# Kernel optimization log

Measured on AMD Instinct MI355X. Metric: run time of the kernel, lower is better.

The kernel has to match this reference:

```python
import jax, jax.numpy as jnp
import numpy as np

THRESHOLD_IOU = 0.8  # forward default in the original module


def setup_inputs() -> dict:
    key = jax.random.key(0)
    k1, k2, k3, k4 = jax.random.split(key, 4)
    N = M = 16
    H = W = 768
    # Binary masks (the original zeroes pixels to 0.0 and tests >0 via torch.where)
    masks_a = (jax.random.uniform(k1, (N, H, W)) > 0.6).astype(jnp.float32)
    masks_b = (jax.random.uniform(k2, (M, H, W)) > 0.6).astype(jnp.float32)
    # Make a few masks identical across labels so the IoU>threshold (suppression)
    # branch is exercised, not just the partial-overlap zeroing branch.
    masks_b = masks_b.at[:4].set(masks_a[:4])
    scores_a = jax.random.uniform(k3, (N,))
    scores_b = jax.random.uniform(k4, (M,))
    return {"masks_a": masks_a, "masks_b": masks_b,
            "scores_a": scores_a, "scores_b": scores_b}


def _overlap_filter(masks_a, masks_b, scores_a, scores_b, thr):
    # Sequential pairwise IoU + overlap zeroing, faithful to the original
    # nested product(enumerate(masks), enumerate(other_masks)) loop order
    # (i outer, j inner), where each pair sees masks already modified by
    # earlier pairs. Pruning ("keep") is applied after the loop; here it is
    # represented with static shapes as keep flags + zeroed-out rows.
    N, H, W = masks_a.shape
    M = masks_b.shape[0]
    P = H * W
    A0 = masks_a.reshape(N, P)
    B0 = masks_b.reshape(M, P)

    def body(carry, k):
        A, B, fi, fj = carry
        i = k // M
        j = k % M
        a = A[i]  # [P]
        b = B[j]  # [P]
        abin = a > 0
        bbin = b > 0
        inter = abin & bbin
        inter_sum = jnp.sum(inter.astype(jnp.float32))
        union_sum = jnp.sum((abin | bbin).astype(jnp.float32))
        iou = inter_sum / jnp.maximum(union_sum, 1.0)
        a_wins = scores_a[i] > scores_b[j]
        suppress = iou > thr                 # mark whole loser mask for removal
        zero_case = (iou > 0) & ~suppress    # zero overlapped pixels of loser
        b_new = jnp.where(zero_case & a_wins & inter, 0.0, b)
        a_new = jnp.where(zero_case & (~a_wins) & inter, 0.0, a)
        A = A.at[i].set(a_new)
        B = B.at[j].set(b_new)
        fj = fj.at[j].set(fj[j] | (suppress & a_wins))
        fi = fi.at[i].set(fi[i] | (suppress & ~a_wins))
        return (A, B, fi, fj), None

    fi0 = jnp.zeros(N, dtype=bool)
    fj0 = jnp.zeros(M, dtype=bool)
    (A, B, fi, fj), _ = jax.lax.scan(body, (A0, B0, fi0, fj0), jnp.arange(N * M))
    keep_a = ~fi
    keep_b = ~fj
    A = jnp.where(keep_a[:, None], A, 0.0)
    B = jnp.where(keep_b[:, None], B, 0.0)
    return A.reshape(N, H, W), B.reshape(M, H, W), keep_a, keep_b


def reference(masks_a, masks_b, scores_a, scores_b):
    return _overlap_filter(masks_a, masks_b, scores_a, scores_b, THRESHOLD_IOU)
```

## Files before the change

kernel.cpp:

```cpp
#include <hip/hip_runtime.h>
#include <stdint.h>

#define NM 16
#define HW_P 589824
#define U8PM 9216
#define C4PM 4608
#define F4PM 147456
#define F4PT 2359296
#define PT 512
#define NG 8
#define EWG 64

typedef unsigned long long u64;
typedef float vf4 __attribute__((ext_vector_type(4)));


__device__ __forceinline__ unsigned aload(const unsigned* p) {
    return __hip_atomic_load(p, __ATOMIC_RELAXED, __HIP_MEMORY_SCOPE_AGENT);
}
__device__ __forceinline__ void astore(unsigned* p, unsigned v) {
    __hip_atomic_store(p, v, __ATOMIC_RELAXED, __HIP_MEMORY_SCOPE_AGENT);
}
__device__ __forceinline__ unsigned afadd(unsigned* p, unsigned v) {
    return __hip_atomic_fetch_add(p, v, __ATOMIC_RELAXED, __HIP_MEMORY_SCOPE_AGENT);
}

#define LOAD16_SC0(dst, addr) \
    asm volatile("global_load_dwordx4 %0, %1, off sc0" : "=v"(dst) : "v"(addr))

__device__ __forceinline__ uint32_t spread4(uint32_t x) {
    uint32_t t = (x | (x << 12)) & 0x000F000Fu;
    t = (t | (t << 6)) & 0x03030303u;
    t = (t | (t << 3)) & 0x11111111u;
    return t;
}

__global__ __launch_bounds__(256) void binarize_kernel(
    const float* __restrict__ ma, const float* __restrict__ mb,
    uint32_t* __restrict__ bitsA, uint32_t* __restrict__ bitsB,
    uint4* __restrict__ meta4)
{
    if (blockIdx.x == 0) {
        uint4 z; z.x = z.y = z.z = z.w = 0u;
        meta4[threadIdx.x] = z;
        meta4[threadIdx.x + 256] = z;
        meta4[threadIdx.x + 512] = z;
        meta4[threadIdx.x + 768] = z;
    }
    int g = blockIdx.x * 256 + threadIdx.x;
    int tensor = (g >= F4PT);
    int lg = tensor ? (g - F4PT) : g;
    const float* src = tensor ? mb : ma;
    vf4 v = __builtin_nontemporal_load(((const vf4*)src) + lg);
    u64 q0 = __ballot(v.x > 0.0f);
    u64 q1 = __ballot(v.y > 0.0f);
    u64 q2 = __ballot(v.z > 0.0f);
    u64 q3 = __ballot(v.w > 0.0f);
    int lane = threadIdx.x & 63;
    if (lane < 8) {
        uint32_t wd = spread4((uint32_t)(q0 >> (8 * lane)) & 0xFFu)
                    | (spread4((uint32_t)(q1 >> (8 * lane)) & 0xFFu) << 1)
                    | (spread4((uint32_t)(q2 >> (8 * lane)) & 0xFFu) << 2)
                    | (spread4((uint32_t)(q3 >> (8 * lane)) & 0xFFu) << 3);
        uint32_t* bits = tensor ? bitsB : bitsA;
        bits[((lg & ~63) >> 3) + lane] = wd;
    }
}

__global__ __launch_bounds__(PT, 1) void pipeline_kernel(
    const float* __restrict__ sa, const float* __restrict__ sb,
    uint32_t* bitsA, uint32_t* bitsB, unsigned* meta, u64* msg)
{
    unsigned* cnt    = meta;
    unsigned* winner = meta + 8;
    int* flagsA      = (int*)(meta + 16);
    int* flagsB      = (int*)(meta + 32);
    unsigned* ackF   = meta + 64;
    unsigned* prodF  = meta + 512;

    const int tid = threadIdx.x;
    const int wave = tid >> 6, lane = tid & 63;

    __shared__ int s_g;
    __shared__ int4 part[2][8];

    if (tid == 0) {
        int xcc;
        asm volatile("s_getreg_b32 %0, hwreg(HW_REG_XCC_ID)" : "=s"(xcc));
        xcc &= 7;
        unsigned slot = afadd(&cnt[xcc], 1u);
        int mine = -1;
        if (slot < NG) {
            if (slot == NG - 1) {
                unsigned exp = 0u;
                __hip_atomic_compare_exchange_strong(
                    winner, &exp, (unsigned)(xcc + 1),
                    __ATOMIC_RELAXED, __ATOMIC_RELAXED, __HIP_MEMORY_SCOPE_AGENT);
            }
            unsigned w;
            while (!(w = aload(winner))) __builtin_amdgcn_s_sleep(1);
            if (w == (unsigned)(xcc + 1)) mine = (int)slot;
        }
        s_g = mine;
    }
    __syncthreads();
    const int g = s_g;
    if (g < 0) return;

    const int c0 = 2 * g, c1 = 2 * g + 1;
    uint4* A4 = (uint4*)bitsA;
    uint4* B4 = (uint4*)bitsB;
    unsigned* ackO = ackF + (g * 8 + wave) * 4;
    unsigned* ackI = ackF + ((g - 1) * 8 + wave) * 4;

    u64 b0[18], b1[18];

    int v0 = 0, v1 = 0;
#pragma unroll
    for (int w = 0; w < 9; ++w) {
        uint4 q0 = B4[(size_t)c0 * C4PM + tid + PT * w];
        uint4 q1 = B4[(size_t)c1 * C4PM + tid + PT * w];
        b0[2 * w] = ((u64)q0.y << 32) | q0.x; b0[2 * w + 1] = ((u64)q0.w << 32) | q0.z;
        b1[2 * w] = ((u64)q1.y << 32) | q1.x; b1[2 * w + 1] = ((u64)q1.w << 32) | q1.z;
        v0 += __popcll(b0[2 * w]) + __popcll(b0[2 * w + 1]);
        v1 += __popcll(b1[2 * w]) + __popcll(b1[2 * w + 1]);
    }
#pragma unroll
    for (int off = 32; off >= 1; off >>= 1) {
        v0 += __shfl_xor(v0, off); v1 += __shfl_xor(v1, off);
    }
    if (lane == 0) { int4 p; p.x = v0; p.y = v1; p.z = 0; p.w = 0; part[0][wave] = p; }
    __syncthreads();
    int pcb0 = 0, pcb1 = 0;
#pragma unroll
    for (int w = 0; w < 8; ++w) { pcb0 += part[0][w].x; pcb1 += part[0][w].y; }
    float sb0 = sb[c0], sb1 = sb[c1];
    int fb0 = 0, fb1 = 0;
    __syncthreads();

    for (int t = 0; t < NM; ++t) {
        int pca, fa;
        uint4 q[9];

        if (g == 0) {
            pca = 0; fa = 0;
#pragma unroll
            for (int w = 0; w < 9; ++w)
                q[w] = A4[(size_t)t * C4PM + tid + PT * w];
        } else {
            const unsigned* fptr = &prodF[(((g - 1) * 16 + t) * 8 + wave) * 4];
            unsigned v;
            do { v = aload(fptr); } while (!v);
            asm volatile("" ::: "memory");
            pca = (int)((v >> 1) & 0xFFFFFu);
            fa  = (int)((v >> 21) & 1u);
            const uint4* s4 = (const uint4*)(msg + (size_t)((g - 1) * 2 + (t & 1)) * U8PM);
#pragma unroll
            for (int w = 0; w < 9; ++w)
                LOAD16_SC0(q[w], s4 + tid + PT * w);
            asm volatile("s_waitcnt vmcnt(0)" ::: "memory");
            __builtin_amdgcn_sched_barrier(0);
            if (lane == 0) astore(ackI, (unsigned)(t + 1));
        }
        u64 a[18];
#pragma unroll
        for (int w = 0; w < 9; ++w) {
            a[2 * w]     = ((u64)q[w].y << 32) | q[w].x;
            a[2 * w + 1] = ((u64)q[w].w << 32) | q[w].z;
        }

        int i0 = 0, i1 = 0, itr = 0, ipc = 0;
#pragma unroll
        for (int w = 0; w < 18; ++w) {
            u64 ab0 = a[w] & b0[w];
            i0 += __popcll(ab0);
            i1 += __popcll(a[w] & b1[w]);
            itr += __popcll(ab0 & b1[w]);
        }
        if (g == 0) {
#pragma unroll
            for (int w = 0; w < 18; ++w) ipc += __popcll(a[w]);
        }
#pragma unroll
        for (int off = 32; off >= 1; off >>= 1) {
            i0 += __shfl_xor(i0, off); i1 += __shfl_xor(i1, off);
            itr += __shfl_xor(itr, off); ipc += __shfl_xor(ipc, off);
        }
        if (lane == 0) {
            int4 p; p.x = i0; p.y = i1; p.z = itr; p.w = ipc;
            part[t & 1][wave] = p;
        }
        __syncthreads();
        int I0 = 0, I1 = 0, T = 0, PC = 0;
#pragma unroll
        for (int w = 0; w < 8; ++w) {
            int4 p = part[t & 1][w];
            I0 += p.x; I1 += p.y; T += p.z; PC += p.w;
        }
        if (g == 0) pca = PC;

        float sai = sa[t];
        bool aupd = false;
        {
            int inter = I0;
            int uni = pca + pcb0 - inter;
            float iou = (float)inter / fmaxf((float)uni, 1.0f);
            bool aw = sai > sb0;
            if (iou > 0.8f) { if (aw) fb0 = 1; else fa = 1; }
            else if (inter > 0) {
                if (aw) {
                    pcb0 -= inter;
#pragma unroll
                    for (int w = 0; w < 18; ++w) b0[w] &= ~a[w];
                } else {
                    pca -= inter; aupd = true;
#pragma unroll
                    for (int w = 0; w < 18; ++w) a[w] &= ~b0[w];
                }
            }
        }
        {
            int inter = aupd ? (I1 - T) : I1;
            int uni = pca + pcb1 - inter;
            float iou = (float)inter / fmaxf((float)uni, 1.0f);
            bool aw = sai > sb1;
            if (iou > 0.8f) { if (aw) fb1 = 1; else fa = 1; }
            else if (inter > 0) {
                if (aw) {
                    pcb1 -= inter;
#pragma unroll
                    for (int w = 0; w < 18; ++w) b1[w] &= ~a[w];
                } else {
                    pca -= inter;
#pragma unroll
                    for (int w = 0; w < 18; ++w) a[w] &= ~b1[w];
                }
            }
        }

        if (g < NG - 1) {
            if (t >= 2) {
                while ((int)aload(ackO) < t - 1) {}
            }
            asm volatile("" ::: "memory");
            uint4* so = (uint4*)(msg + (size_t)(g * 2 + (t & 1)) * U8PM);
#pragma unroll
            for (int w = 0; w < 9; ++w) {
                uint4 o;
                o.x = (uint32_t)a[2 * w];     o.y = (uint32_t)(a[2 * w] >> 32);
                o.z = (uint32_t)a[2 * w + 1]; o.w = (uint32_t)(a[2 * w + 1] >> 32);
                so[tid + PT * w] = o;
            }
            asm volatile("s_waitcnt vmcnt(0)" ::: "memory");
            if (lane == 0)
                astore(&prodF[((g * 16 + t) * 8 + wave) * 4],
                       1u | ((unsigned)pca << 1) | ((unsigned)fa << 21));
        } else {
            uint4* Ar = A4 + (size_t)t * C4PM;
#pragma unroll
            for (int w = 0; w < 9; ++w) {
                uint4 o;
                o.x = (uint32_t)a[2 * w];     o.y = (uint32_t)(a[2 * w] >> 32);
                o.z = (uint32_t)a[2 * w + 1]; o.w = (uint32_t)(a[2 * w + 1] >> 32);
                Ar[tid + PT * w] = o;
            }
            if (tid == 0) flagsA[t] = fa;
        }
    }

    uint4* Wc0 = B4 + (size_t)c0 * C4PM;
    uint4* Wc1 = B4 + (size_t)c1 * C4PM;
#pragma unroll
    for (int w = 0; w < 9; ++w) {
        uint4 q0, q1;
        q0.x = (uint32_t)b0[2 * w];     q0.y = (uint32_t)(b0[2 * w] >> 32);
        q0.z = (uint32_t)b0[2 * w + 1]; q0.w = (uint32_t)(b0[2 * w + 1] >> 32);
        q1.x = (uint32_t)b1[2 * w];     q1.y = (uint32_t)(b1[2 * w] >> 32);
        q1.z = (uint32_t)b1[2 * w + 1]; q1.w = (uint32_t)(b1[2 * w + 1] >> 32);
        Wc0[tid + PT * w] = q0;
        Wc1[tid + PT * w] = q1;
    }
    if (tid == 0) { flagsB[c0] = fb0; flagsB[c1] = fb1; }
}

__global__ __launch_bounds__(256) void expand_kernel(
    const uint32_t* __restrict__ bitsA, const uint32_t* __restrict__ bitsB,
    const int* __restrict__ meta, float* __restrict__ out)
{
    int g = blockIdx.x * 256 + threadIdx.x;
    int tensor = (g >= F4PT);
    int lg = tensor ? (g - F4PT) : g;
    const uint32_t* bits = tensor ? bitsB : bitsA;
    const int* flags = meta + (tensor ? 32 : 16);
    int m = lg / F4PM;
    bool keep = (flags[m] == 0);
    uint32_t wd = keep ? bits[lg >> 3] : 0u;
    int sh = (lg & 7) * 4;
    vf4 o;
    o.x = ((wd >> (sh + 0)) & 1u) ? 1.0f : 0.0f;
    o.y = ((wd >> (sh + 1)) & 1u) ? 1.0f : 0.0f;
    o.z = ((wd >> (sh + 2)) & 1u) ? 1.0f : 0.0f;
    o.w = ((wd >> (sh + 3)) & 1u) ? 1.0f : 0.0f;
    __builtin_nontemporal_store(o, ((vf4*)out) + g);
    if (g < 2 * NM) {
        out[(size_t)2 * NM * HW_P + g] = meta[16 + g] ? 0.0f : 1.0f;
    }
}

extern "C" void kernel_launch(void* const* d_in, const int* in_sizes, int n_in,
                              void* d_out, int out_size, void* d_ws, size_t ws_size,
                              hipStream_t stream)
{
    const float* ma = (const float*)d_in[0];
    const float* mb = (const float*)d_in[1];
    const float* sa = (const float*)d_in[2];
    const float* sb = (const float*)d_in[3];
    float* out = (float*)d_out;
    char* ws = (char*)d_ws;

    uint32_t* bitsA = (uint32_t*)(ws);
    uint32_t* bitsB = (uint32_t*)(ws + 1179648);
    unsigned* meta  = (unsigned*)(ws + 2359296);
    u64* msg        = (u64*)(ws + 2375680);

    binarize_kernel<<<18432, 256, 0, stream>>>(ma, mb, bitsA, bitsB,
                                               (uint4*)meta);
    pipeline_kernel<<<EWG, PT, 0, stream>>>(sa, sb, bitsA, bitsB, meta, msg);
    expand_kernel<<<18432, 256, 0, stream>>>(bitsA, bitsB, (const int*)meta, out);
}
```

Before: 227.5 us.

## Split each pipeline stage across four workgroups with atomic count reduction

Each of the 8 pipeline stages (owning two B masks) is now handled by 4 workgroups of 256 threads, each owning a quarter-slice of the bit masks, instead of one 512-thread workgroup. The per-step intersection and popcount partials are combined across the 4 slices through packed 64-bit atomic adds in global memory, with each slice spinning until all 4 have contributed. The per-slice handoff flags and acks are re-indexed to match. This aims to spread the per-step bit work and memory traffic over more CUs, at the cost of an extra cross-workgroup atomic rendezvous on every step.

Result: slower. 246.5 us (+8.3%).

```diff
diff --git a/kernel.cpp b/kernel.cpp
--- a/kernel.cpp
+++ b/kernel.cpp
@@ -4,12 +4,14 @@
 #define NM 16
 #define HW_P 589824
 #define U8PM 9216
-#define C4PM 4608
+#define SLC 2304
 #define F4PM 147456
 #define F4PT 2359296
-#define PT 512
+#define PT 256
 #define NG 8
-#define EWG 64
+#define NS 4
+#define NWIN 32
+#define EWG 256
 
 typedef unsigned long long u64;
 typedef float vf4 __attribute__((ext_vector_type(4)));
@@ -24,9 +26,15 @@
 __device__ __forceinline__ unsigned afadd(unsigned* p, unsigned v) {
     return __hip_atomic_fetch_add(p, v, __ATOMIC_RELAXED, __HIP_MEMORY_SCOPE_AGENT);
 }
-
-#define LOAD16_SC0(dst, addr) \
-    asm volatile("global_load_dwordx4 %0, %1, off sc0" : "=v"(dst) : "v"(addr))
+__device__ __forceinline__ u64 aload64(const u64* p) {
+    return __hip_atomic_load(p, __ATOMIC_RELAXED, __HIP_MEMORY_SCOPE_AGENT);
+}
+__device__ __forceinline__ void afadd64(u64* p, u64 v) {
+    (void)__hip_atomic_fetch_add(p, v, __ATOMIC_RELAXED, __HIP_MEMORY_SCOPE_AGENT);
+}
+
+#define LOAD8_SC0(dst, addr) \
+    asm volatile("global_load_dwordx2 %0, %1, off sc0" : "=v"(dst) : "v"(addr))
 
 __device__ __forceinline__ uint32_t spread4(uint32_t x) {
     uint32_t t = (x | (x << 12)) & 0x000F000Fu;
@@ -42,10 +50,9 @@
 {
     if (blockIdx.x == 0) {
         uint4 z; z.x = z.y = z.z = z.w = 0u;
-        meta4[threadIdx.x] = z;
-        meta4[threadIdx.x + 256] = z;
-        meta4[threadIdx.x + 512] = z;
-        meta4[threadIdx.x + 768] = z;
+#pragma unroll
+        for (int i = 0; i < 8; ++i)
+            meta4[threadIdx.x + 256 * i] = z;
     }
     int g = blockIdx.x * 256 + threadIdx.x;
     int tensor = (g >= F4PT);
@@ -75,14 +82,12 @@
     unsigned* winner = meta + 8;
     int* flagsA      = (int*)(meta + 16);
     int* flagsB      = (int*)(meta + 32);
-    unsigned* ackF   = meta + 64;
-    unsigned* prodF  = meta + 512;
 
     const int tid = threadIdx.x;
     const int wave = tid >> 6, lane = tid & 63;
 
-    __shared__ int s_g;
-    __shared__ int4 part[2][8];
+    __shared__ int s_gs;
+    __shared__ int4 part[2][4];
 
     if (tid == 0) {
         int xcc;
@@ -90,8 +95,8 @@
         xcc &= 7;
         unsigned slot = afadd(&cnt[xcc], 1u);
         int mine = -1;
-        if (slot < NG) {
-            if (slot == NG - 1) {
+        if (slot < NWIN) {
+            if (slot == NWIN - 1) {
                 unsigned exp = 0u;
                 __hip_atomic_compare_exchange_strong(
                     winner, &exp, (unsigned)(xcc + 1),
@@ -101,29 +106,28 @@
             while (!(w = aload(winner))) __builtin_amdgcn_s_sleep(1);
             if (w == (unsigned)(xcc + 1)) mine = (int)slot;
         }
-        s_g = mine;
+        s_gs = mine;
     }
     __syncthreads();
-    const int g = s_g;
-    if (g < 0) return;
+    const int gs = s_gs;
+    if (gs < 0) return;
+    const int g = gs >> 2, s = gs & 3;
 
     const int c0 = 2 * g, c1 = 2 * g + 1;
-    uint4* A4 = (uint4*)bitsA;
-    uint4* B4 = (uint4*)bitsB;
-    unsigned* ackO = ackF + (g * 8 + wave) * 4;
-    unsigned* ackI = ackF + ((g - 1) * 8 + wave) * 4;
-
-    u64 b0[18], b1[18];
+    const u64* A64 = (const u64*)bitsA;
+    u64* B64 = (u64*)bitsB;
+    const int soff = s * SLC + tid;
+    unsigned* ackO = meta + 192 + g * 16 + s * 4 + wave;
+    unsigned* ackI = meta + 192 + (g - 1) * 16 + s * 4 + wave;
+
+    u64 b0[9], b1[9];
 
     int v0 = 0, v1 = 0;
 #pragma unroll
-    for (int w = 0; w < 9; ++w) {
-        uint4 q0 = B4[(size_t)c0 * C4PM + tid + PT * w];
-        uint4 q1 = B4[(size_t)c1 * C4PM + tid + PT * w];
-        b0[2 * w] = ((u64)q0.y << 32) | q0.x; b0[2 * w + 1] = ((u64)q0.w << 32) | q0.z;
-        b1[2 * w] = ((u64)q1.y << 32) | q1.x; b1[2 * w + 1] = ((u64)q1.w << 32) | q1.z;
-        v0 += __popcll(b0[2 * w]) + __popcll(b0[2 * w + 1]);
-        v1 += __popcll(b1[2 * w]) + __popcll(b1[2 * w + 1]);
+    for (int k = 0; k < 9; ++k) {
+        b0[k] = B64[(size_t)c0 * U8PM + soff + 256 * k];
+        b1[k] = B64[(size_t)c1 * U8PM + soff + 256 * k];
+        v0 += __popcll(b0[k]); v1 += __popcll(b1[k]);
     }
 #pragma unroll
     for (int off = 32; off >= 1; off >>= 1) {
@@ -131,55 +135,56 @@
     }
     if (lane == 0) { int4 p; p.x = v0; p.y = v1; p.z = 0; p.w = 0; part[0][wave] = p; }
     __syncthreads();
-    int pcb0 = 0, pcb1 = 0;
-#pragma unroll
-    for (int w = 0; w < 8; ++w) { pcb0 += part[0][w].x; pcb1 += part[0][w].y; }
+    int wv0 = 0, wv1 = 0;
+#pragma unroll
+    for (int w = 0; w < 4; ++w) { wv0 += part[0][w].x; wv1 += part[0][w].y; }
+    u64* a0p = (u64*)(meta + 64 + g * 16);
+    if (tid == 0)
+        afadd64(a0p, (1ull << 48) | ((u64)wv1 << 24) | (u64)wv0);
+    u64 iv;
+    do { iv = aload64(a0p); } while ((iv >> 48) != NS);
+    int pcb0 = (int)(iv & 0xFFFFFFu);
+    int pcb1 = (int)((iv >> 24) & 0xFFFFFFu);
     float sb0 = sb[c0], sb1 = sb[c1];
     int fb0 = 0, fb1 = 0;
     __syncthreads();
 
     for (int t = 0; t < NM; ++t) {
         int pca, fa;
-        uint4 q[9];
+        u64 a[9];
 
         if (g == 0) {
             pca = 0; fa = 0;
 #pragma unroll
-            for (int w = 0; w < 9; ++w)
-                q[w] = A4[(size_t)t * C4PM + tid + PT * w];
+            for (int k = 0; k < 9; ++k)
+                a[k] = A64[(size_t)t * U8PM + soff + 256 * k];
         } else {
-            const unsigned* fptr = &prodF[(((g - 1) * 16 + t) * 8 + wave) * 4];
+            const unsigned* fptr = meta + 320 + ((g - 1) * 16 + t) * 16 + s * 4 + wave;
             unsigned v;
             do { v = aload(fptr); } while (!v);
             asm volatile("" ::: "memory");
             pca = (int)((v >> 1) & 0xFFFFFu);
             fa  = (int)((v >> 21) & 1u);
-            const uint4* s4 = (const uint4*)(msg + (size_t)((g - 1) * 2 + (t & 1)) * U8PM);
-#pragma unroll
-            for (int w = 0; w < 9; ++w)
-                LOAD16_SC0(q[w], s4 + tid + PT * w);
+            const u64* srcp = msg + (size_t)((g - 1) * 2 + (t & 1)) * U8PM + soff;
+#pragma unroll
+            for (int k = 0; k < 9; ++k)
+                LOAD8_SC0(a[k], srcp + 256 * k);
             asm volatile("s_waitcnt vmcnt(0)" ::: "memory");
             __builtin_amdgcn_sched_barrier(0);
             if (lane == 0) astore(ackI, (unsigned)(t + 1));
         }
-        u64 a[18];
-#pragma unroll
-        for (int w = 0; w < 9; ++w) {
-            a[2 * w]     = ((u64)q[w].y << 32) | q[w].x;
-            a[2 * w + 1] = ((u64)q[w].w << 32) | q[w].z;
-        }
 
         int i0 = 0, i1 = 0, itr = 0, ipc = 0;
 #pragma unroll
-        for (int w = 0; w < 18; ++w) {
-            u64 ab0 = a[w] & b0[w];
+        for (int k = 0; k < 9; ++k) {
+            u64 ab0 = a[k] & b0[k];
             i0 += __popcll(ab0);
-            i1 += __popcll(a[w] & b1[w]);
-            itr += __popcll(ab0 & b1[w]);
+            i1 += __popcll(a[k] & b1[k]);
+            itr += __popcll(ab0 & b1[k]);
         }
         if (g == 0) {
 #pragma unroll
-            for (int w = 0; w < 18; ++w) ipc += __popcll(a[w]);
+            for (int k = 0; k < 9; ++k) ipc += __popcll(a[k]);
         }
 #pragma unroll
         for (int off = 32; off >= 1; off >>= 1) {
@@ -193,10 +198,22 @@
         __syncthreads();
         int I0 = 0, I1 = 0, T = 0, PC = 0;
 #pragma unroll
-        for (int w = 0; w < 8; ++w) {
+        for (int w = 0; w < 4; ++w) {
             int4 p = part[t & 1][w];
             I0 += p.x; I1 += p.y; T += p.z; PC += p.w;
         }
+
+        u64* accA = (u64*)(meta + 2112 + (g * 16 + t) * 16);
+        u64* accB = accA + 1;
+        if (tid == 0) {
+            afadd64(accB, (1ull << 48) | ((u64)PC << 24) | (u64)T);
+            afadd64(accA, (1ull << 48) | ((u64)I1 << 24) | (u64)I0);
+        }
+        u64 va, vb;
+        do { va = aload64(accA); } while ((va >> 48) != NS);
+        do { vb = aload64(accB); } while ((vb >> 48) != NS);
+        I0 = (int)(va & 0xFFFFFFu); I1 = (int)((va >> 24) & 0xFFFFFFu);
+        T  = (int)(vb & 0xFFFFFFu); PC = (int)((vb >> 24) & 0xFFFFFFu);
         if (g == 0) pca = PC;
 
         float sai = sa[t];
@@ -211,11 +228,11 @@
                 if (aw) {
                     pcb0 -= inter;
 #pragma unroll
-                    for (int w = 0; w < 18; ++w) b0[w] &= ~a[w];
+                    for (int k = 0; k < 9; ++k) b0[k] &= ~a[k];
                 } else {
                     pca -= inter; aupd = true;
 #pragma unroll
-                    for (int w = 0; w < 18; ++w) a[w] &= ~b0[w];
+                    for (int k = 0; k < 9; ++k) a[k] &= ~b0[k];
                 }
             }
         }
@@ -229,11 +246,11 @@
                 if (aw) {
                     pcb1 -= inter;
 #pragma unroll
-                    for (int w = 0; w < 18; ++w) b1[w] &= ~a[w];
+                    for (int k = 0; k < 9; ++k) b1[k] &= ~a[k];
                 } else {
                     pca -= inter;
 #pragma unroll
-                    for (int w = 0; w < 18; ++w) a[w] &= ~b1[w];
+                    for (int k = 0; k < 9; ++k) a[k] &= ~b1[k];
                 }
             }
         }
@@ -243,44 +260,29 @@
                 while ((int)aload(ackO) < t - 1) {}
             }
             asm volatile("" ::: "memory");
-            uint4* so = (uint4*)(msg + (size_t)(g * 2 + (t & 1)) * U8PM);
-#pragma unroll
-            for (int w = 0; w < 9; ++w) {
-                uint4 o;
-                o.x = (uint32_t)a[2 * w];     o.y = (uint32_t)(a[2 * w] >> 32);
-                o.z = (uint32_t)a[2 * w + 1]; o.w = (uint32_t)(a[2 * w + 1] >> 32);
-                so[tid + PT * w] = o;
-            }
+            u64* dst = msg + (size_t)(g * 2 + (t & 1)) * U8PM + soff;
+#pragma unroll
+            for (int k = 0; k < 9; ++k)
+                dst[256 * k] = a[k];
             asm volatile("s_waitcnt vmcnt(0)" ::: "memory");
             if (lane == 0)
-                astore(&prodF[((g * 16 + t) * 8 + wave) * 4],
+                astore(meta + 320 + (g * 16 + t) * 16 + s * 4 + wave,
                        1u | ((unsigned)pca << 1) | ((unsigned)fa << 21));
         } else {
-            uint4* Ar = A4 + (size_t)t * C4PM;
-#pragma unroll
-            for (int w = 0; w < 9; ++w) {
-                uint4 o;
-                o.x = (uint32_t)a[2 * w];     o.y = (uint32_t)(a[2 * w] >> 32);
-                o.z = (uint32_t)a[2 * w + 1]; o.w = (uint32_t)(a[2 * w + 1] >> 32);
-                Ar[tid + PT * w] = o;
-            }
-            if (tid == 0) flagsA[t] = fa;
-        }
-    }
-
-    uint4* Wc0 = B4 + (size_t)c0 * C4PM;
-    uint4* Wc1 = B4 + (size_t)c1 * C4PM;
-#pragma unroll
-    for (int w = 0; w < 9; ++w) {
-        uint4 q0, q1;
-        q0.x = (uint32_t)b0[2 * w];     q0.y = (uint32_t)(b0[2 * w] >> 32);
-        q0.z = (uint32_t)b0[2 * w + 1]; q0.w = (uint32_t)(b0[2 * w + 1] >> 32);
-        q1.x = (uint32_t)b1[2 * w];     q1.y = (uint32_t)(b1[2 * w] >> 32);
-        q1.z = (uint32_t)b1[2 * w + 1]; q1.w = (uint32_t)(b1[2 * w + 1] >> 32);
-        Wc0[tid + PT * w] = q0;
-        Wc1[tid + PT * w] = q1;
-    }
-    if (tid == 0) { flagsB[c0] = fb0; flagsB[c1] = fb1; }
+            u64* dst = (u64*)bitsA + (size_t)t * U8PM + soff;
+#pragma unroll
+            for (int k = 0; k < 9; ++k)
+                dst[256 * k] = a[k];
+            if (s == 0 && tid == 0) flagsA[t] = fa;
+        }
+    }
+
+#pragma unroll
+    for (int k = 0; k < 9; ++k) {
+        B64[(size_t)c0 * U8PM + soff + 256 * k] = b0[k];
+        B64[(size_t)c1 * U8PM + soff + 256 * k] = b1[k];
+    }
+    if (s == 0 && tid == 0) { flagsB[c0] = fb0; flagsB[c1] = fb1; }
 }
 
 __global__ __launch_bounds__(256) void expand_kernel(
@@ -321,7 +323,7 @@
     uint32_t* bitsA = (uint32_t*)(ws);
     uint32_t* bitsB = (uint32_t*)(ws + 1179648);
     unsigned* meta  = (unsigned*)(ws + 2359296);
-    u64* msg        = (u64*)(ws + 2375680);
+    u64* msg        = (u64*)(ws + 2392064);
 
     binarize_kernel<<<18432, 256, 0, stream>>>(ma, mb, bitsA, bitsB,
                                                (uint4*)meta);
```
